# Optimization experiments

Hardware: AMD Instinct MI355X
Metric: run time of the kernel (lower is better)

Reference implementation:

```python
import jax, jax.numpy as jnp
import numpy as np
from math import sqrt

N_NODES = 50000
N_EDGES = 800000
NUM_RADIAL = 6
HIDDEN = 128
FACTOR2 = HIDDEN // 2  # factor*2 = hidden/2


def swish(v):
    return v * jax.nn.sigmoid(v)


def setup_inputs() -> dict:
    key = jax.random.key(0)
    ks = jax.random.split(key, 9)
    s3 = sqrt(3.0)
    x = jax.random.randint(ks[0], (N_NODES, 2), 0, 20, dtype=jnp.int64)
    rbf = jax.random.normal(ks[1], (N_EDGES, NUM_RADIAL), dtype=jnp.float32)
    i = jax.random.randint(ks[2], (N_EDGES,), 0, N_NODES, dtype=jnp.int64)
    j = jax.random.randint(ks[3], (N_EDGES,), 0, N_NODES, dtype=jnp.int64)
    resi_emb_w = jax.random.uniform(ks[4], (20, FACTOR2), jnp.float32, -s3, s3)
    atom_emb_w = jax.random.uniform(ks[5], (95, FACTOR2), jnp.float32, -s3, s3)
    # torch Linear default init: U(-1/sqrt(fan_in), 1/sqrt(fan_in))
    b1 = 1.0 / sqrt(NUM_RADIAL)
    W_rbf = jax.random.uniform(ks[6], (HIDDEN, NUM_RADIAL), jnp.float32, -b1, b1)
    b_rbf = jax.random.uniform(ks[7], (HIDDEN,), jnp.float32, -b1, b1)
    b2 = 1.0 / sqrt(3 * HIDDEN)
    kA, kB = jax.random.split(ks[8])
    W_lin = jax.random.uniform(kA, (HIDDEN, 3 * HIDDEN), jnp.float32, -b2, b2)
    b_lin = jax.random.uniform(kB, (HIDDEN,), jnp.float32, -b2, b2)
    return {"x": x, "rbf": rbf, "i": i, "j": j,
            "resi_emb_w": resi_emb_w, "atom_emb_w": atom_emb_w,
            "W_rbf": W_rbf, "b_rbf": b_rbf, "W_lin": W_lin, "b_lin": b_lin}


def reference(x, rbf, i, j, resi_emb_w, atom_emb_w, W_rbf, b_rbf, W_lin, b_lin):
    # node features: concat of residue and atom embeddings -> [N, hidden]
    node = jnp.concatenate([resi_emb_w[x[:, 0]], atom_emb_w[x[:, 1]]], axis=-1)
    # rbf projection + swish -> [E, hidden]
    rbf_h = swish(rbf @ W_rbf.T + b_rbf)
    # edge-wise gather + concat + linear + swish -> [E, hidden]
    h = jnp.concatenate([node[i], node[j], rbf_h], axis=-1)
    return swish(h @ W_lin.T + b_lin)
```

## Files before the change

### kernel.cpp

```cpp
#include <hip/hip_runtime.h>
#include <hip/hip_bf16.h>
#include <hip/hip_fp16.h>

typedef _Float16 f16x8 __attribute__((ext_vector_type(8)));
typedef __fp16   h16x2 __attribute__((ext_vector_type(2)));
typedef float    f32x4 __attribute__((ext_vector_type(4)));

#define KDIM     384
#define MBLK     64
#define PADK     392
#define NEDGE    800000
#define WP_ELEMS 49152

__device__ __forceinline__ float fast_swish(float v) {
  return v * __builtin_amdgcn_rcpf(1.0f + __expf(-v));
}

__device__ __forceinline__ void pack8(_Float16* dst, float4 a, float4 b) {
  union { h16x2 h[4]; f16x8 v; } u;
  u.h[0] = __builtin_amdgcn_cvt_pkrtz(a.x, a.y);
  u.h[1] = __builtin_amdgcn_cvt_pkrtz(a.z, a.w);
  u.h[2] = __builtin_amdgcn_cvt_pkrtz(b.x, b.y);
  u.h[3] = __builtin_amdgcn_cvt_pkrtz(b.z, b.w);
  *(f16x8*)dst = u.v;
}

__global__ void pack_w_kernel(const float* __restrict__ W_lin,
                              const float* __restrict__ W_rbf,
                              _Float16* __restrict__ Wp,
                              _Float16* __restrict__ Wrp) {
  int idx = blockIdx.x * 256 + threadIdx.x;
  if (idx < WP_ELEMS) {
    int e  = idx & 7;
    int l  = (idx >> 3) & 63;
    int nt = (idx >> 9) & 7;
    int ks = idx >> 12;
    int n  = (nt << 4) + (l & 15);
    int k  = (ks << 5) + ((l >> 4) << 3) + e;
    Wp[idx] = (_Float16)W_lin[n * KDIM + k];
  } else if (idx < WP_ELEMS + 4096) {
    int idx2 = idx - WP_ELEMS;
    int e  = idx2 & 7;
    int l  = (idx2 >> 3) & 63;
    int nt = idx2 >> 9;
    int k  = ((l >> 4) << 3) + e;
    float v = (k < 6) ? W_rbf[(nt * 16 + (l & 15)) * 6 + k] : 0.0f;
    Wrp[idx2] = (_Float16)v;
  }
}

__global__ __launch_bounds__(256, 3)
void embed_main_kernel(const int* __restrict__ x,
                       const float* __restrict__ rbf,
                       const int* __restrict__ gi,
                       const int* __restrict__ gj,
                       const float* __restrict__ resi_w,
                       const float* __restrict__ atom_w,
                       const float* __restrict__ b_rbf,
                       const float* __restrict__ b_lin,
                       const _Float16* __restrict__ Wp,
                       const _Float16* __restrict__ Wrp,
                       float* __restrict__ out) {
  __shared__ alignas(16) _Float16 hlds[MBLK][PADK];
  const int tid  = threadIdx.x;
  const int e0   = blockIdx.x * MBLK;
  const int lane = tid & 63;
  const int wave = tid >> 6;
  const int g    = lane >> 4;
  const int c    = lane & 15;

  const int cc  = tid & 15;
  const int seg = cc >> 2;
  const int off = (cc & 3) << 4;
  const int* __restrict__ gsel = (seg < 2) ? gi : gj;
  const float* __restrict__ tbl = (seg & 1) ? atom_w : resi_w;
  const int m0 = tid >> 4;
  int sel_[4];
  #pragma unroll
  for (int it = 0; it < 4; ++it) {
    int node = gsel[e0 + m0 + it * 16];
    sel_[it] = x[(node << 1) + (seg & 1)];
  }

  {
    f16x8 ra = {0, 0, 0, 0, 0, 0, 0, 0};
    if (g == 0) {
      const float* rp = rbf + (size_t)(e0 + wave * 16 + c) * 6;
      ra[0] = (_Float16)rp[0]; ra[1] = (_Float16)rp[1]; ra[2] = (_Float16)rp[2];
      ra[3] = (_Float16)rp[3]; ra[4] = (_Float16)rp[4]; ra[5] = (_Float16)rp[5];
    }
    const f16x8* wrb = (const f16x8*)Wrp + lane;
    #pragma unroll
    for (int nt = 0; nt < 8; ++nt) {
      f16x8 rb = wrb[nt * 64];
      f32x4 d = __builtin_amdgcn_mfma_f32_16x16x32_f16(ra, rb,
                  (f32x4){0.f, 0.f, 0.f, 0.f}, 0, 0, 0);
      float bb = b_rbf[nt * 16 + c];
      #pragma unroll
      for (int r = 0; r < 4; ++r) {
        float vv = d[r] + bb;
        hlds[wave * 16 + 4 * g + r][256 + nt * 16 + c] = (_Float16)fast_swish(vv);
      }
    }
  }

  #pragma unroll
  for (int it = 0; it < 4; ++it) {
    int m = m0 + it * 16;
    const float4* s4 = (const float4*)(tbl + sel_[it] * 64 + off);
    float4 v0 = s4[0], v1 = s4[1], v2 = s4[2], v3 = s4[3];
    _Float16* dst = &hlds[m][cc << 4];
    pack8(dst,     v0, v1);
    pack8(dst + 8, v2, v3);
  }
  __syncthreads();

  const _Float16* abase = &hlds[c][g << 3];
  const f16x8* wpB = (const f16x8*)Wp + (wave * 2) * 64 + lane;

  f32x4 acc[4][2];
  #pragma unroll
  for (int mt = 0; mt < 4; ++mt) {
    acc[mt][0] = (f32x4){0.f, 0.f, 0.f, 0.f};
    acc[mt][1] = (f32x4){0.f, 0.f, 0.f, 0.f};
  }

  #pragma unroll
  for (int ks = 0; ks < 12; ++ks) {
    f16x8 b0 = wpB[ks * 512];
    f16x8 b1 = wpB[ks * 512 + 64];
    #pragma unroll
    for (int mt = 0; mt < 4; ++mt) {
      f16x8 a = *(const f16x8*)(abase + mt * 16 * PADK + ks * 32);
      acc[mt][0] = __builtin_amdgcn_mfma_f32_16x16x32_f16(a, b0, acc[mt][0], 0, 0, 0);
      acc[mt][1] = __builtin_amdgcn_mfma_f32_16x16x32_f16(a, b1, acc[mt][1], 0, 0, 0);
    }
  }

  const int col0 = wave * 32 + c;
  const float bl0 = b_lin[col0];
  const float bl1 = b_lin[col0 + 16];
  #pragma unroll
  for (int mt = 0; mt < 4; ++mt) {
    const int erow = e0 + mt * 16 + 4 * g;
    #pragma unroll
    for (int r = 0; r < 4; ++r) {
      float* orow = out + (size_t)(erow + r) * 128;
      orow[col0]      = fast_swish(acc[mt][0][r] + bl0);
      orow[col0 + 16] = fast_swish(acc[mt][1][r] + bl1);
    }
  }
}

extern "C" void kernel_launch(void* const* d_in, const int* in_sizes, int n_in,
                              void* d_out, int out_size, void* d_ws, size_t ws_size,
                              hipStream_t stream) {
  const int*   x      = (const int*)d_in[0];
  const float* rbf    = (const float*)d_in[1];
  const int*   gi     = (const int*)d_in[2];
  const int*   gj     = (const int*)d_in[3];
  const float* resi_w = (const float*)d_in[4];
  const float* atom_w = (const float*)d_in[5];
  const float* W_rbf  = (const float*)d_in[6];
  const float* b_rbf  = (const float*)d_in[7];
  const float* W_lin  = (const float*)d_in[8];
  const float* b_lin  = (const float*)d_in[9];
  float* out = (float*)d_out;
  _Float16* Wp  = (_Float16*)d_ws;
  _Float16* Wrp = (_Float16*)d_ws + WP_ELEMS;

  hipLaunchKernelGGL(pack_w_kernel, dim3(208), dim3(256), 0, stream,
                     W_lin, W_rbf, Wp, Wrp);
  hipLaunchKernelGGL(embed_main_kernel, dim3(NEDGE / MBLK), dim3(256), 0, stream,
                     x, rbf, gi, gj, resi_w, atom_w, b_rbf, b_lin, Wp, Wrp, out);
}
```

Before: 205.5 us.

## Switch main GEMM to 32x32x16 MFMA with register-prefetched weight chunks

The main edge GEMM moves from 16x16x32 MFMA tiles, where each wave covered all 64 rows by 32 columns, to 32x32x16 MFMA tiles, where each wave covers 32 rows by 64 columns. The packed weight layout is changed to match. Weight fragments are now double-buffered in registers, and the first chunk is prefetched before the gather and LDS fill, so global weight loads overlap compute. This should halve LDS A-fragment reads per MFMA and hide weight-load latency. The cost is much higher register pressure from 24 f16x8 buffers plus 32 accumulators, which may hurt occupancy under the 3-block launch bound.

```diff
diff --git a/kernel.cpp b/kernel.cpp
--- a/kernel.cpp
+++ b/kernel.cpp
@@ -2,9 +2,10 @@
 #include <hip/hip_bf16.h>
 #include <hip/hip_fp16.h>
 
-typedef _Float16 f16x8 __attribute__((ext_vector_type(8)));
-typedef __fp16   h16x2 __attribute__((ext_vector_type(2)));
-typedef float    f32x4 __attribute__((ext_vector_type(4)));
+typedef _Float16 f16x8  __attribute__((ext_vector_type(8)));
+typedef __fp16   h16x2  __attribute__((ext_vector_type(2)));
+typedef float    f32x4  __attribute__((ext_vector_type(4)));
+typedef float    f32x16 __attribute__((ext_vector_type(16)));
 
 #define KDIM     384
 #define MBLK     64
@@ -33,10 +34,10 @@
   if (idx < WP_ELEMS) {
     int e  = idx & 7;
     int l  = (idx >> 3) & 63;
-    int nt = (idx >> 9) & 7;
-    int ks = idx >> 12;
-    int n  = (nt << 4) + (l & 15);
-    int k  = (ks << 5) + ((l >> 4) << 3) + e;
+    int nt = (idx >> 9) & 3;
+    int ks = idx >> 11;
+    int n  = nt * 32 + (l & 31);
+    int k  = ks * 16 + ((l >> 5) << 3) + e;
     Wp[idx] = (_Float16)W_lin[n * KDIM + k];
   } else if (idx < WP_ELEMS + 4096) {
     int idx2 = idx - WP_ELEMS;
@@ -66,8 +67,19 @@
   const int e0   = blockIdx.x * MBLK;
   const int lane = tid & 63;
   const int wave = tid >> 6;
-  const int g    = lane >> 4;
-  const int c    = lane & 15;
+  const int m    = wave >> 1;
+  const int nb   = (wave & 1) * 2;
+  const int c5   = lane & 31;
+  const int g2   = lane >> 5;
+
+  const f16x8* wp2 = (const f16x8*)Wp + lane;
+
+  f16x8 breg[2][12];
+  #pragma unroll
+  for (int q = 0; q < 12; ++q) {
+    int ks = q >> 1, ntg = nb + (q & 1);
+    breg[0][q] = wp2[(ks * 4 + ntg) * 64];
+  }
 
   const int cc  = tid & 15;
   const int seg = cc >> 2;
@@ -83,6 +95,8 @@
   }
 
   {
+    const int g = lane >> 4;
+    const int c = lane & 15;
     f16x8 ra = {0, 0, 0, 0, 0, 0, 0, 0};
     if (g == 0) {
       const float* rp = rbf + (size_t)(e0 + wave * 16 + c) * 6;
@@ -106,49 +120,48 @@
 
   #pragma unroll
   for (int it = 0; it < 4; ++it) {
-    int m = m0 + it * 16;
+    int mm = m0 + it * 16;
     const float4* s4 = (const float4*)(tbl + sel_[it] * 64 + off);
     float4 v0 = s4[0], v1 = s4[1], v2 = s4[2], v3 = s4[3];
-    _Float16* dst = &hlds[m][cc << 4];
+    _Float16* dst = &hlds[mm][cc << 4];
     pack8(dst,     v0, v1);
     pack8(dst + 8, v2, v3);
   }
   __syncthreads();
 
-  const _Float16* abase = &hlds[c][g << 3];
-  const f16x8* wpB = (const f16x8*)Wp + (wave * 2) * 64 + lane;
+  const _Float16* abase = &hlds[(m << 5) + c5][g2 << 3];
 
-  f32x4 acc[4][2];
-  #pragma unroll
-  for (int mt = 0; mt < 4; ++mt) {
-    acc[mt][0] = (f32x4){0.f, 0.f, 0.f, 0.f};
-    acc[mt][1] = (f32x4){0.f, 0.f, 0.f, 0.f};
-  }
+  f32x16 acc0 = {};
+  f32x16 acc1 = {};
 
   #pragma unroll
-  for (int ks = 0; ks < 12; ++ks) {
-    f16x8 b0 = wpB[ks * 512];
-    f16x8 b1 = wpB[ks * 512 + 64];
+  for (int chunk = 0; chunk < 4; ++chunk) {
+    if (chunk < 3) {
+      #pragma unroll
+      for (int q = 0; q < 12; ++q) {
+        int ks = (chunk + 1) * 6 + (q >> 1), ntg = nb + (q & 1);
+        breg[(chunk + 1) & 1][q] = wp2[(ks * 4 + ntg) * 64];
+      }
+    }
     #pragma unroll
-    for (int mt = 0; mt < 4; ++mt) {
-      f16x8 a = *(const f16x8*)(abase + mt * 16 * PADK + ks * 32);
-      acc[mt][0] = __builtin_amdgcn_mfma_f32_16x16x32_f16(a, b0, acc[mt][0], 0, 0, 0);
-      acc[mt][1] = __builtin_amdgcn_mfma_f32_16x16x32_f16(a, b1, acc[mt][1], 0, 0, 0);
+    for (int kl = 0; kl < 6; ++kl) {
+      int ks = chunk * 6 + kl;
+      f16x8 a = *(const f16x8*)(abase + ks * 16);
+      acc0 = __builtin_amdgcn_mfma_f32_32x32x16_f16(a, breg[chunk & 1][kl * 2],     acc0, 0, 0, 0);
+      acc1 = __builtin_amdgcn_mfma_f32_32x32x16_f16(a, breg[chunk & 1][kl * 2 + 1], acc1, 0, 0, 0);
     }
   }
 
-  const int col0 = wave * 32 + c;
-  const float bl0 = b_lin[col0];
-  const float bl1 = b_lin[col0 + 16];
+  const int colA = (wave & 1) * 64 + c5;
+  const int colB = colA + 32;
+  const float blA = b_lin[colA];
+  const float blB = b_lin[colB];
   #pragma unroll
-  for (int mt = 0; mt < 4; ++mt) {
-    const int erow = e0 + mt * 16 + 4 * g;
-    #pragma unroll
-    for (int r = 0; r < 4; ++r) {
-      float* orow = out + (size_t)(erow + r) * 128;
-      orow[col0]      = fast_swish(acc[mt][0][r] + bl0);
-      orow[col0 + 16] = fast_swish(acc[mt][1][r] + bl1);
-    }
+  for (int reg = 0; reg < 16; ++reg) {
+    int row = (reg & 3) + 8 * (reg >> 2) + 4 * g2;
+    float* orow = out + (size_t)(e0 + (m << 5) + row) * 128;
+    orow[colA] = fast_swish(acc0[reg] + blA);
+    orow[colB] = fast_swish(acc1[reg] + blB);
   }
 }
 
```

Result: slower. 221.5 us (+7.8%).
